# Performance work log

Hardware: AMD Instinct MI355X
Metric: run time of the kernel (lower is better)

## Reference

```python
import jax, jax.numpy as jnp
import numpy as np

B, T, C = 4, 2048, 1024
H, D = 16, 64  # num_heads, head_size; H*D == C


def setup_inputs() -> dict:
    key = jax.random.key(0)
    k1, k2, k3 = jax.random.split(key, 3)
    x = jax.random.normal(k1, (B, T, C), dtype=jnp.float32)
    w_qkv = jax.random.normal(k2, (C, 3 * C), dtype=jnp.float32) * (C ** -0.5)
    w_out = jax.random.normal(k3, (C, C), dtype=jnp.float32) * (C ** -0.5)
    b_out = jnp.zeros((C,), dtype=jnp.float32)
    return {"x": x, "w_qkv": w_qkv, "w_out": w_out, "b_out": b_out}


def reference(x, w_qkv, w_out, b_out):
    Bb, Tt, Cc = x.shape
    qkv = x @ w_qkv                        # [B,T,3C]
    q, k, v = jnp.split(qkv, 3, axis=2)
    # [B,T,C] -> [B,H,T,D]
    q = q.reshape(Bb, Tt, H, D).transpose(0, 2, 1, 3)
    k = k.reshape(Bb, Tt, H, D).transpose(0, 2, 1, 3)
    v = v.reshape(Bb, Tt, H, D).transpose(0, 2, 1, 3)
    scores = jnp.einsum('bhqd,bhkd->bhqk', q, k) * (D ** -0.5)
    causal = jnp.tril(jnp.ones((Tt, Tt), dtype=bool))
    scores = jnp.where(causal, scores, -jnp.inf)
    attn = jax.nn.softmax(scores, axis=-1)  # dropout is identity in eval mode
    out = jnp.einsum('bhqk,bhkd->bhqd', attn, v)
    out = out.transpose(0, 2, 1, 3).reshape(Bb, Tt, Cc)
    return out @ w_out + b_out
```

## Files before the change

### kernel.cpp

```cpp
#include <hip/hip_runtime.h>

typedef __bf16 bf16;
typedef __bf16 bf16x4 __attribute__((ext_vector_type(4)));
typedef __bf16 bf16x8 __attribute__((ext_vector_type(8)));
typedef float  f32x4  __attribute__((ext_vector_type(4)));

#define MFMA16(A_, B_, C_) __builtin_amdgcn_mfma_f32_16x16x32_bf16((A_), (B_), (C_), 0, 0, 0)

#define BB 4
#define TT 2048
#define CC 1024
#define HH 16
#define DD 64
#define MM (BB * TT)
#define N_QKV (3 * CC)
#define LDSS 68
#define BSTRIDE 36
#define QSCALE2 0.18033688f

static __device__ __forceinline__ void store_lds8(bf16* p, bf16x8 v) {
  bf16x4 lo, hi;
#pragma unroll
  for (int i = 0; i < 4; i++) { lo[i] = v[i]; hi[i] = v[i + 4]; }
  *(bf16x4*)p = lo;
  *(bf16x4*)(p + 4) = hi;
}

static __device__ __forceinline__ bf16x8 load_lds8(const bf16* p) {
  bf16x4 lo = *(const bf16x4*)p;
  bf16x4 hi = *(const bf16x4*)(p + 4);
  bf16x8 v;
#pragma unroll
  for (int i = 0; i < 4; i++) { v[i] = lo[i]; v[i + 4] = hi[i]; }
  return v;
}

static __device__ __forceinline__ void async_cp16(const bf16* g, bf16* l) {
  __builtin_amdgcn_global_load_lds(
      (const __attribute__((address_space(1))) void*)g,
      (__attribute__((address_space(3))) void*)l, 16, 0, 0);
}

__global__ __launch_bounds__(256) void sniff_k(const unsigned short* __restrict__ u,
                                               int* __restrict__ flag) {
  __shared__ int s;
  if (threadIdx.x == 0) s = 0;
  __syncthreads();
  int c = 0;
  for (int i = threadIdx.x; i < 65536; i += 256)
    if ((u[i] & 0x7F80u) == 0x7F80u) c = 1;
  if (c) atomicOr(&s, 1);
  __syncthreads();
  if (threadIdx.x == 0) *flag = s;
}

__global__ __launch_bounds__(256) void cvt_k(const void* __restrict__ in,
                                             bf16* __restrict__ out,
                                             const int* __restrict__ flag) {
  const int fl = *flag;
  const size_t i = ((size_t)blockIdx.x * 256 + threadIdx.x) * 8;
  if (fl) {
    f32x4 a = *(const f32x4*)((const float*)in + i);
    f32x4 b = *(const f32x4*)((const float*)in + i + 4);
    bf16x8 o;
#pragma unroll
    for (int j = 0; j < 4; j++) { o[j] = (bf16)a[j]; o[4 + j] = (bf16)b[j]; }
    *(bf16x8*)(out + i) = o;
  } else {
    *(bf16x8*)(out + i) = *(const bf16x8*)((const bf16*)in + i);
  }
}

__global__ __launch_bounds__(256) void transpose_k(const void* __restrict__ in,
                                                   bf16* __restrict__ out,
                                                   int R, int C,
                                                   const int* __restrict__ flag) {
  __shared__ bf16 tile[32][33];
  const int fl = *flag;
  const int c0 = blockIdx.x * 32, r0 = blockIdx.y * 32;
  const int tx = threadIdx.x & 31, ty = threadIdx.x >> 5;
#pragma unroll
  for (int i = ty; i < 32; i += 8) {
    const size_t idx = (size_t)(r0 + i) * C + c0 + tx;
    tile[i][tx] = fl ? (bf16)((const float*)in)[idx] : ((const bf16*)in)[idx];
  }
  __syncthreads();
#pragma unroll
  for (int i = ty; i < 32; i += 8)
    out[(size_t)(c0 + i) * R + r0 + tx] = tile[tx][i];
}

template <int EPI>
__global__ __launch_bounds__(256) void gemm_lds(const bf16* __restrict__ A,
                                                const bf16* __restrict__ Bt,
                                                const void* __restrict__ biasv,
                                                void* __restrict__ Cv,
                                                const int* __restrict__ flag,
                                                size_t aoff, size_t coff,
                                                int M, int N, int K,
                                                int lda, int ldc) {
  const int fl = *flag;
  __shared__ __align__(16) bf16 sA[128 * 32];
  __shared__ __align__(16) bf16 sB[128 * 32];
  const int tid = threadIdx.x;
  const int lane = tid & 63, wave = tid >> 6;
  const int quad = lane >> 4, l15 = lane & 15;
  const int wr = wave >> 1, wc = wave & 1;
  const int m0 = blockIdx.x * 128, n0 = blockIdx.y * 128;
  const int grow = lane >> 2;
  const int gcol = (lane & 3) * 8;

  f32x4 acc[4][4];
#pragma unroll
  for (int i = 0; i < 4; i++)
#pragma unroll
    for (int j = 0; j < 4; j++) {
      f32x4 z = {0.f, 0.f, 0.f, 0.f};
      acc[i][j] = z;
    }

  const bf16* Ag = A + aoff + (size_t)(m0 + wave * 32 + grow) * lda + gcol;
  const bf16* Bg = Bt + (size_t)(n0 + wave * 32 + grow) * K + gcol;
  bf16* sAw = sA + wave * 32 * 32;
  bf16* sBw = sB + wave * 32 * 32;

  for (int k0 = 0; k0 < K; k0 += 32) {
    __syncthreads();
    async_cp16(Ag, sAw);
    async_cp16(Ag + (size_t)16 * lda, sAw + 16 * 32);
    async_cp16(Bg, sBw);
    async_cp16(Bg + (size_t)16 * K, sBw + 16 * 32);
    Ag += 32;
    Bg += 32;
    __syncthreads();

    bf16x8 af[4], bfr[4];
#pragma unroll
    for (int mi = 0; mi < 4; mi++)
      af[mi] = *(const bf16x8*)(sA + (wr * 64 + mi * 16 + l15) * 32 + quad * 8);
#pragma unroll
    for (int ni = 0; ni < 4; ni++)
      bfr[ni] = *(const bf16x8*)(sB + (wc * 64 + ni * 16 + l15) * 32 + quad * 8);
#pragma unroll
    for (int mi = 0; mi < 4; mi++)
#pragma unroll
      for (int ni = 0; ni < 4; ni++)
        acc[mi][ni] = MFMA16(af[mi], bfr[ni], acc[mi][ni]);
  }

#pragma unroll
  for (int mi = 0; mi < 4; mi++) {
#pragma unroll
    for (int r = 0; r < 4; r++) {
      const int m = m0 + wr * 64 + mi * 16 + quad * 4 + r;
#pragma unroll
      for (int ni = 0; ni < 4; ni++) {
        const int n = n0 + wc * 64 + ni * 16 + l15;
        float v = acc[mi][ni][r];
        const size_t idx = coff + (size_t)m * ldc + n;
        if (EPI == 1) {
          v += fl ? ((const float*)biasv)[n] : (float)((const bf16*)biasv)[n];
          if (fl) ((float*)Cv)[idx] = v;
          else    ((bf16*)Cv)[idx] = (bf16)v;
        } else {
          ((bf16*)Cv)[idx] = (bf16)v;
        }
      }
    }
  }
}

template <int EPI, bool AF>
__global__ __launch_bounds__(256) void gemm_bt(const void* __restrict__ Av,
                                               const bf16* __restrict__ Bt,
                                               const void* __restrict__ biasv,
                                               void* __restrict__ Cv,
                                               const int* __restrict__ flag,
                                               size_t aoff, size_t coff,
                                               int M, int N, int K,
                                               int lda, int ldc) {
  const int fl = *flag;
  const bool af32 = AF && (fl != 0);
  __shared__ __align__(16) bf16 sA[128 * 32];
  __shared__ __align__(16) bf16 sB[128 * 32];
  const int tid = threadIdx.x;
  const int lane = tid & 63, wave = tid >> 6;
  const int quad = lane >> 4, l15 = lane & 15;
  const int wr = wave >> 1, wc = wave & 1;
  const int m0 = blockIdx.x * 128, n0 = blockIdx.y * 128;
  const int srow = tid >> 2;
  const int scol = (tid & 3) * 8;

  f32x4 acc[4][4];
#pragma unroll
  for (int i = 0; i < 4; i++)
#pragma unroll
    for (int j = 0; j < 4; j++) {
      f32x4 z = {0.f, 0.f, 0.f, 0.f};
      acc[i][j] = z;
    }

  const size_t abase0 = aoff + (size_t)(m0 + srow) * lda + scol;
  const size_t abase1 = abase0 + (size_t)64 * lda;
  const bf16* Bg0 = Bt + (size_t)(n0 + srow) * K + scol;
  const bf16* Bg1 = Bg0 + (size_t)64 * K;

  for (int k0 = 0; k0 < K; k0 += 32) {
    bf16x8 a0, a1;
    if (af32) {
      const float* Af = (const float*)Av;
      f32x4 p00 = *(const f32x4*)(Af + abase0 + k0);
      f32x4 p01 = *(const f32x4*)(Af + abase0 + k0 + 4);
      f32x4 p10 = *(const f32x4*)(Af + abase1 + k0);
      f32x4 p11 = *(const f32x4*)(Af + abase1 + k0 + 4);
#pragma unroll
      for (int i = 0; i < 4; i++) {
        a0[i] = (bf16)p00[i]; a0[i + 4] = (bf16)p01[i];
        a1[i] = (bf16)p10[i]; a1[i + 4] = (bf16)p11[i];
      }
    } else {
      const bf16* Ab = (const bf16*)Av;
      a0 = *(const bf16x8*)(Ab + abase0 + k0);
      a1 = *(const bf16x8*)(Ab + abase1 + k0);
    }
    bf16x8 b0 = *(const bf16x8*)(Bg0 + k0);
    bf16x8 b1 = *(const bf16x8*)(Bg1 + k0);
    __syncthreads();
    *(bf16x8*)(sA + srow * 32 + scol) = a0;
    *(bf16x8*)(sA + (64 + srow) * 32 + scol) = a1;
    *(bf16x8*)(sB + srow * 32 + scol) = b0;
    *(bf16x8*)(sB + (64 + srow) * 32 + scol) = b1;
    __syncthreads();

    bf16x8 af[4], bfr[4];
#pragma unroll
    for (int mi = 0; mi < 4; mi++)
      af[mi] = *(const bf16x8*)(sA + (wr * 64 + mi * 16 + l15) * 32 + quad * 8);
#pragma unroll
    for (int ni = 0; ni < 4; ni++)
      bfr[ni] = *(const bf16x8*)(sB + (wc * 64 + ni * 16 + l15) * 32 + quad * 8);
#pragma unroll
    for (int mi = 0; mi < 4; mi++)
#pragma unroll
      for (int ni = 0; ni < 4; ni++)
        acc[mi][ni] = MFMA16(af[mi], bfr[ni], acc[mi][ni]);
  }

#pragma unroll
  for (int mi = 0; mi < 4; mi++) {
#pragma unroll
    for (int r = 0; r < 4; r++) {
      const int m = m0 + wr * 64 + mi * 16 + quad * 4 + r;
#pragma unroll
      for (int ni = 0; ni < 4; ni++) {
        const int n = n0 + wc * 64 + ni * 16 + l15;
        float v = acc[mi][ni][r];
        const size_t idx = coff + (size_t)m * ldc + n;
        if (EPI == 1) {
          v += fl ? ((const float*)biasv)[n] : (float)((const bf16*)biasv)[n];
          if (fl) ((float*)Cv)[idx] = v;
          else    ((bf16*)Cv)[idx] = (bf16)v;
        } else {
          ((bf16*)Cv)[idx] = (bf16)v;
        }
      }
    }
  }
}

template <int EPI, bool AF, bool WF>
__global__ __launch_bounds__(256) void gemm_nt(const void* __restrict__ Av,
                                               const void* __restrict__ Wv,
                                               const void* __restrict__ biasv,
                                               void* __restrict__ Cv,
                                               const int* __restrict__ flag,
                                               size_t aoff, size_t coff,
                                               int M, int N, int K,
                                               int lda, int ldc) {
  const int fl = *flag;
  const bool af32 = AF && (fl != 0);
  const bool wf32 = WF && (fl != 0);
  __shared__ __align__(16) bf16 sA[128 * 32];
  __shared__ __align__(16) bf16 sB[128 * BSTRIDE];
  const int tid = threadIdx.x;
  const int lane = tid & 63, wave = tid >> 6;
  const int quad = lane >> 4, l15 = lane & 15;
  const int wr = wave >> 1, wc = wave & 1;
  const int m0 = blockIdx.x * 128, n0 = blockIdx.y * 128;
  const int arow = tid >> 2, acol = (tid & 3) * 8;
  const int wk = tid >> 3, wn = (tid & 7) * 16;

  f32x4 acc[4][4];
#pragma unroll
  for (int i = 0; i < 4; i++)
#pragma unroll
    for (int j = 0; j < 4; j++) {
      f32x4 z = {0.f, 0.f, 0.f, 0.f};
      acc[i][j] = z;
    }

  const size_t abase0 = aoff + (size_t)(m0 + arow) * lda + acol;
  const size_t abase1 = abase0 + (size_t)64 * lda;

  for (int k0 = 0; k0 < K; k0 += 32) {
    bf16x8 a0, a1;
    if (af32) {
      const float* Af = (const float*)Av;
      f32x4 p00 = *(const f32x4*)(Af + abase0 + k0);
      f32x4 p01 = *(const f32x4*)(Af + abase0 + k0 + 4);
      f32x4 p10 = *(const f32x4*)(Af + abase1 + k0);
      f32x4 p11 = *(const f32x4*)(Af + abase1 + k0 + 4);
#pragma unroll
      for (int i = 0; i < 4; i++) {
        a0[i] = (bf16)p00[i]; a0[i + 4] = (bf16)p01[i];
        a1[i] = (bf16)p10[i]; a1[i + 4] = (bf16)p11[i];
      }
    } else {
      const bf16* Ab = (const bf16*)Av;
      a0 = *(const bf16x8*)(Ab + abase0 + k0);
      a1 = *(const bf16x8*)(Ab + abase1 + k0);
    }
    bf16 wreg[16];
    const size_t wbase = (size_t)(k0 + wk) * N + n0 + wn;
    if (wf32) {
      const float* Wf = (const float*)Wv;
      f32x4 q0 = *(const f32x4*)(Wf + wbase);
      f32x4 q1 = *(const f32x4*)(Wf + wbase + 4);
      f32x4 q2 = *(const f32x4*)(Wf + wbase + 8);
      f32x4 q3 = *(const f32x4*)(Wf + wbase + 12);
#pragma unroll
      for (int i = 0; i < 4; i++) {
        wreg[i] = (bf16)q0[i];      wreg[4 + i] = (bf16)q1[i];
        wreg[8 + i] = (bf16)q2[i];  wreg[12 + i] = (bf16)q3[i];
      }
    } else {
      const bf16* Wb = (const bf16*)Wv;
      bf16x8 w0 = *(const bf16x8*)(Wb + wbase);
      bf16x8 w1 = *(const bf16x8*)(Wb + wbase + 8);
#pragma unroll
      for (int i = 0; i < 8; i++) { wreg[i] = w0[i]; wreg[8 + i] = w1[i]; }
    }
    __syncthreads();
    *(bf16x8*)(sA + arow * 32 + acol) = a0;
    *(bf16x8*)(sA + (64 + arow) * 32 + acol) = a1;
#pragma unroll
    for (int i = 0; i < 16; i++)
      sB[(wn + i) * BSTRIDE + wk] = wreg[i];
    __syncthreads();

    bf16x8 af[4], bfr[4];
#pragma unroll
    for (int mi = 0; mi < 4; mi++)
      af[mi] = *(const bf16x8*)(sA + (wr * 64 + mi * 16 + l15) * 32 + quad * 8);
#pragma unroll
    for (int ni = 0; ni < 4; ni++)
      bfr[ni] = load_lds8(sB + (wc * 64 + ni * 16 + l15) * BSTRIDE + quad * 8);
#pragma unroll
    for (int mi = 0; mi < 4; mi++)
#pragma unroll
      for (int ni = 0; ni < 4; ni++)
        acc[mi][ni] = MFMA16(af[mi], bfr[ni], acc[mi][ni]);
  }

#pragma unroll
  for (int mi = 0; mi < 4; mi++) {
#pragma unroll
    for (int r = 0; r < 4; r++) {
      const int m = m0 + wr * 64 + mi * 16 + quad * 4 + r;
#pragma unroll
      for (int ni = 0; ni < 4; ni++) {
        const int n = n0 + wc * 64 + ni * 16 + l15;
        float v = acc[mi][ni][r];
        const size_t idx = coff + (size_t)m * ldc + n;
        if (EPI == 1) {
          v += fl ? ((const float*)biasv)[n] : (float)((const bf16*)biasv)[n];
          if (fl) ((float*)Cv)[idx] = v;
          else    ((bf16*)Cv)[idx] = (bf16)v;
        } else {
          ((bf16*)Cv)[idx] = (bf16)v;
        }
      }
    }
  }
}

__global__ __launch_bounds__(256) void attn_k(bf16* __restrict__ qkv) {
  __shared__ __align__(16) bf16 sQ[128 * LDSS];
  __shared__ __align__(16) bf16 sK[64 * LDSS];
  __shared__ __align__(16) bf16 sVt[64 * LDSS];

  const int tid = threadIdx.x;
  const int lane = tid & 63, wave = tid >> 6;
  const int quad = lane >> 4, l15 = lane & 15;
  const int bh = blockIdx.y;
  bf16* base = qkv + (size_t)(bh >> 4) * TT * N_QKV + (bh & 15) * DD;
  const bf16* Qp = base;
  const bf16* Kp = base + CC;
  const bf16* Vp = base + 2 * CC;

  const int krow = tid >> 2;
  const int kcol = (tid & 3) * 16;
  const int vkey = tid & 31;
  const int vcol = (tid >> 5) * 8;

  bf16x8 ones;
  {
    const bf16 o = (l15 == 0) ? (bf16)1.0f : (bf16)0.0f;
#pragma unroll
    for (int i = 0; i < 8; i++) ones[i] = o;
  }

  for (int pass = 0; pass < 2; pass++) {
    const int qt = pass ? (15 - (int)blockIdx.x) : (int)blockIdx.x;
    const int q0 = qt * 128;
    __syncthreads();

#pragma unroll
    for (int p = 0; p < 2; p++) {
      const int r = p * 64 + krow;
      const bf16* src = Qp + (size_t)(q0 + r) * N_QKV + kcol;
      bf16x8 v0 = *(const bf16x8*)src;
      bf16x8 v1 = *(const bf16x8*)(src + 8);
#pragma unroll
      for (int i = 0; i < 8; i++) {
        v0[i] = (bf16)((float)v0[i] * QSCALE2);
        v1[i] = (bf16)((float)v1[i] * QSCALE2);
      }
      store_lds8(sQ + r * LDSS + kcol, v0);
      store_lds8(sQ + r * LDSS + kcol + 8, v1);
    }

    bf16x8 kr0, kr1, vr0, vr1;
    {
      const bf16* kp = Kp + (size_t)krow * N_QKV + kcol;
      kr0 = *(const bf16x8*)kp;
      kr1 = *(const bf16x8*)(kp + 8);
      vr0 = *(const bf16x8*)(Vp + (size_t)vkey * N_QKV + vcol);
      vr1 = *(const bf16x8*)(Vp + (size_t)(32 + vkey) * N_QKV + vcol);
    }
    __syncthreads();

    bf16x8 aq[2][2];
#pragma unroll
    for (int mi = 0; mi < 2; mi++) {
      const bf16* qp = sQ + (size_t)(wave * 32 + mi * 16 + l15) * LDSS + quad * 8;
      aq[mi][0] = load_lds8(qp);
      aq[mi][1] = load_lds8(qp + 32);
    }

    f32x4 Oacc[2][4];
    f32x4 lacc[2];
#pragma unroll
    for (int mi = 0; mi < 2; mi++) {
      f32x4 z = {0.f, 0.f, 0.f, 0.f};
      lacc[mi] = z;
#pragma unroll
      for (int nt = 0; nt < 4; nt++) Oacc[mi][nt] = z;
    }

    const int jmax = q0 + 64;
    const int wave_row0 = q0 + wave * 32;
    bf16* sP = sQ + (size_t)(wave * 32) * LDSS;

    for (int j0 = 0; j0 <= jmax; j0 += 64) {
      __syncthreads();
      store_lds8(sK + krow * LDSS + kcol, kr0);
      store_lds8(sK + krow * LDSS + kcol + 8, kr1);
#pragma unroll
      for (int i = 0; i < 8; i++) {
        sVt[(vcol + i) * LDSS + vkey] = vr0[i];
        sVt[(vcol + i) * LDSS + 32 + vkey] = vr1[i];
      }
      __syncthreads();

      if (j0 + 64 <= jmax) {
        const bf16* kp = Kp + (size_t)(j0 + 64 + krow) * N_QKV + kcol;
        kr0 = *(const bf16x8*)kp;
        kr1 = *(const bf16x8*)(kp + 8);
        vr0 = *(const bf16x8*)(Vp + (size_t)(j0 + 64 + vkey) * N_QKV + vcol);
        vr1 = *(const bf16x8*)(Vp + (size_t)(j0 + 96 + vkey) * N_QKV + vcol);
      }

      if (j0 <= wave_row0 + 31) {
        f32x4 S[2][4];
#pragma unroll
        for (int nt = 0; nt < 4; nt++) {
          const bf16* kp = sK + (size_t)(nt * 16 + l15) * LDSS + quad * 8;
          bf16x8 bk0 = load_lds8(kp);
          bf16x8 bk1 = load_lds8(kp + 32);
#pragma unroll
          for (int mi = 0; mi < 2; mi++) {
            f32x4 acc = {0.f, 0.f, 0.f, 0.f};
            acc = MFMA16(aq[mi][0], bk0, acc);
            acc = MFMA16(aq[mi][1], bk1, acc);
            S[mi][nt] = acc;
          }
        }

        if (j0 + 63 > wave_row0) {
#pragma unroll
          for (int mi = 0; mi < 2; mi++)
#pragma unroll
            for (int nt = 0; nt < 4; nt++) {
              const int kc = j0 + nt * 16 + l15;
#pragma unroll
              for (int r = 0; r < 4; r++) {
                const float e = __builtin_amdgcn_exp2f(S[mi][nt][r]);
                const bool dead = kc > wave_row0 + mi * 16 + quad * 4 + r;
                sP[(size_t)(mi * 16 + quad * 4 + r) * LDSS + nt * 16 + l15] =
                    (bf16)(dead ? 0.f : e);
              }
            }
        } else {
#pragma unroll
          for (int mi = 0; mi < 2; mi++)
#pragma unroll
            for (int nt = 0; nt < 4; nt++)
#pragma unroll
              for (int r = 0; r < 4; r++)
                sP[(size_t)(mi * 16 + quad * 4 + r) * LDSS + nt * 16 + l15] =
                    (bf16)__builtin_amdgcn_exp2f(S[mi][nt][r]);
        }

        bf16x8 ap[2][2];
#pragma unroll
        for (int mi = 0; mi < 2; mi++) {
          const bf16* pp = sP + (size_t)(mi * 16 + l15) * LDSS + quad * 8;
          ap[mi][0] = load_lds8(pp);
          ap[mi][1] = load_lds8(pp + 32);
          lacc[mi] = MFMA16(ap[mi][0], ones, lacc[mi]);
          lacc[mi] = MFMA16(ap[mi][1], ones, lacc[mi]);
        }
#pragma unroll
        for (int nt = 0; nt < 4; nt++) {
          const bf16* vp = sVt + (size_t)(nt * 16 + l15) * LDSS + quad * 8;
          bf16x8 bv0 = load_lds8(vp);
          bf16x8 bv1 = load_lds8(vp + 32);
#pragma unroll
          for (int mi = 0; mi < 2; mi++) {
            Oacc[mi][nt] = MFMA16(ap[mi][0], bv0, Oacc[mi][nt]);
            Oacc[mi][nt] = MFMA16(ap[mi][1], bv1, Oacc[mi][nt]);
          }
        }
      }
    }

#pragma unroll
    for (int mi = 0; mi < 2; mi++)
#pragma unroll
      for (int r = 0; r < 4; r++) {
        const float lv = __shfl(lacc[mi][r], lane & 48, 64);
        const float invl = 1.0f / lv;
        const int t = q0 + wave * 32 + mi * 16 + quad * 4 + r;
#pragma unroll
        for (int nt = 0; nt < 4; nt++)
          base[(size_t)t * N_QKV + nt * 16 + l15] =
              (bf16)(Oacc[mi][nt][r] * invl);
      }
  }
}

extern "C" void kernel_launch(void* const* d_in, const int* in_sizes, int n_in,
                              void* d_out, int out_size, void* d_ws, size_t ws_size,
                              hipStream_t stream) {
  const void* x = d_in[0];
  const void* w_qkv = d_in[1];
  const void* w_out = d_in[2];
  const void* b_out = d_in[3];

  int* flag = (int*)d_ws;
  char* p = (char*)d_ws + 256;
  bf16* wqkvT = (bf16*)p;
  bf16* woutT = wqkvT + (size_t)N_QKV * CC;

  const size_t wT_bytes = ((size_t)N_QKV * CC + (size_t)CC * CC) * 2;
  const size_t xb_bytes = (size_t)MM * CC * 2;
  const size_t qkv_bytes = (size_t)MM * N_QKV * 2;
  const size_t need_Ap = 256 + wT_bytes + xb_bytes + qkv_bytes;
  const size_t need_A  = 256 + wT_bytes + qkv_bytes;
  const size_t need_B  = 256 + wT_bytes + (size_t)TT * N_QKV * 2;

  sniff_k<<<1, 256, 0, stream>>>((const unsigned short*)x, flag);

  if (ws_size >= need_Ap) {
    bf16* xb = woutT + (size_t)CC * CC;
    bf16* qkv = xb + (size_t)MM * CC;
    cvt_k<<<(MM * CC) / 2048, 256, 0, stream>>>(x, xb, flag);
    transpose_k<<<dim3(N_QKV / 32, CC / 32), 256, 0, stream>>>(w_qkv, wqkvT, CC, N_QKV, flag);
    transpose_k<<<dim3(CC / 32, CC / 32), 256, 0, stream>>>(w_out, woutT, CC, CC, flag);

    gemm_lds<0><<<dim3(MM / 128, N_QKV / 128), 256, 0, stream>>>(
        xb, wqkvT, nullptr, qkv, flag, 0, 0, MM, N_QKV, CC, CC, N_QKV);

    attn_k<<<dim3(8, BB * HH), 256, 0, stream>>>(qkv);

    gemm_lds<1><<<dim3(MM / 128, CC / 128), 256, 0, stream>>>(
        qkv, woutT, b_out, d_out, flag, 0, 0, MM, CC, CC, N_QKV, CC);
  } else if (ws_size >= need_A) {
    bf16* qkv = woutT + (size_t)CC * CC;
    transpose_k<<<dim3(N_QKV / 32, CC / 32), 256, 0, stream>>>(w_qkv, wqkvT, CC, N_QKV, flag);
    transpose_k<<<dim3(CC / 32, CC / 32), 256, 0, stream>>>(w_out, woutT, CC, CC, flag);

    gemm_bt<0, true><<<dim3(MM / 128, N_QKV / 128), 256, 0, stream>>>(
        x, wqkvT, nullptr, qkv, flag, 0, 0, MM, N_QKV, CC, CC, N_QKV);

    attn_k<<<dim3(8, BB * HH), 256, 0, stream>>>(qkv);

    gemm_lds<1><<<dim3(MM / 128, CC / 128), 256, 0, stream>>>(
        qkv, woutT, b_out, d_out, flag, 0, 0, MM, CC, CC, N_QKV, CC);
  } else if (ws_size >= need_B) {
    bf16* qkv = woutT + (size_t)CC * CC;
    transpose_k<<<dim3(N_QKV / 32, CC / 32), 256, 0, stream>>>(w_qkv, wqkvT, CC, N_QKV, flag);
    transpose_k<<<dim3(CC / 32, CC / 32), 256, 0, stream>>>(w_out, woutT, CC, CC, flag);
    for (int b = 0; b < BB; b++) {
      const size_t xoff = (size_t)b * TT * CC;
      gemm_bt<0, true><<<dim3(TT / 128, N_QKV / 128), 256, 0, stream>>>(
          x, wqkvT, nullptr, qkv, flag, xoff, 0, TT, N_QKV, CC, CC, N_QKV);
      attn_k<<<dim3(8, HH), 256, 0, stream>>>(qkv);
      gemm_lds<1><<<dim3(TT / 128, CC / 128), 256, 0, stream>>>(
          qkv, woutT, b_out, d_out, flag, 0, xoff, TT, CC, CC, N_QKV, CC);
    }
  } else {
    bf16* qkvb = (bf16*)p;
    for (int b = 0; b < BB; b++) {
      const size_t xoff = (size_t)b * TT * CC;
      gemm_nt<0, true, true><<<dim3(TT / 128, N_QKV / 128), 256, 0, stream>>>(
          x, w_qkv, nullptr, qkvb, flag, xoff, 0, TT, N_QKV, CC, CC, N_QKV);
      attn_k<<<dim3(8, HH), 256, 0, stream>>>(qkvb);
      gemm_nt<1, false, true><<<dim3(TT / 128, CC / 128), 256, 0, stream>>>(
          qkvb, w_out, b_out, d_out, flag, 0, xoff, TT, CC, CC, N_QKV, CC);
    }
  }
}
```

Before: 332.6 us.

## Pad attention LDS rows to 72 and use 16-byte LDS accesses; chunk x conversion

Widens the attention shared-memory row stride from 68 to 72 bf16 so rows stay 16-byte aligned, letting the split 8-byte LDS loads and stores be replaced by single 16-byte vector accesses. The two causal-mask branches are merged into one loop with a runtime mask predicate. The host path now reorders workspace so that, when there is too little room for a full bf16 copy of x, it converts and multiplies x in half-size chunks instead of falling back to the direct fp32 GEMM. The wider stride uses more LDS and can change bank-conflict patterns, and the merged mask loop adds a compare on unmasked tiles.

```diff
diff --git a/kernel.cpp b/kernel.cpp
--- a/kernel.cpp
+++ b/kernel.cpp
@@ -14,7 +14,7 @@
 #define DD 64
 #define MM (BB * TT)
 #define N_QKV (3 * CC)
-#define LDSS 68
+#define LDSS 72
 #define BSTRIDE 36
 #define QSCALE2 0.18033688f
 
@@ -56,18 +56,19 @@
 
 __global__ __launch_bounds__(256) void cvt_k(const void* __restrict__ in,
                                              bf16* __restrict__ out,
-                                             const int* __restrict__ flag) {
+                                             const int* __restrict__ flag,
+                                             size_t off) {
   const int fl = *flag;
   const size_t i = ((size_t)blockIdx.x * 256 + threadIdx.x) * 8;
   if (fl) {
-    f32x4 a = *(const f32x4*)((const float*)in + i);
-    f32x4 b = *(const f32x4*)((const float*)in + i + 4);
+    f32x4 a = *(const f32x4*)((const float*)in + off + i);
+    f32x4 b = *(const f32x4*)((const float*)in + off + i + 4);
     bf16x8 o;
 #pragma unroll
     for (int j = 0; j < 4; j++) { o[j] = (bf16)a[j]; o[4 + j] = (bf16)b[j]; }
     *(bf16x8*)(out + i) = o;
   } else {
-    *(bf16x8*)(out + i) = *(const bf16x8*)((const bf16*)in + i);
+    *(bf16x8*)(out + i) = *(const bf16x8*)((const bf16*)in + off + i);
   }
 }
 
@@ -426,8 +427,8 @@
         v0[i] = (bf16)((float)v0[i] * QSCALE2);
         v1[i] = (bf16)((float)v1[i] * QSCALE2);
       }
-      store_lds8(sQ + r * LDSS + kcol, v0);
-      store_lds8(sQ + r * LDSS + kcol + 8, v1);
+      *(bf16x8*)(sQ + r * LDSS + kcol) = v0;
+      *(bf16x8*)(sQ + r * LDSS + kcol + 8) = v1;
     }
 
     bf16x8 kr0, kr1, vr0, vr1;
@@ -444,8 +445,8 @@
 #pragma unroll
     for (int mi = 0; mi < 2; mi++) {
       const bf16* qp = sQ + (size_t)(wave * 32 + mi * 16 + l15) * LDSS + quad * 8;
-      aq[mi][0] = load_lds8(qp);
-      aq[mi][1] = load_lds8(qp + 32);
+      aq[mi][0] = *(const bf16x8*)qp;
+      aq[mi][1] = *(const bf16x8*)(qp + 32);
     }
 
     f32x4 Oacc[2][4];
@@ -464,8 +465,8 @@
 
     for (int j0 = 0; j0 <= jmax; j0 += 64) {
       __syncthreads();
-      store_lds8(sK + krow * LDSS + kcol, kr0);
-      store_lds8(sK + krow * LDSS + kcol + 8, kr1);
+      *(bf16x8*)(sK + krow * LDSS + kcol) = kr0;
+      *(bf16x8*)(sK + krow * LDSS + kcol + 8) = kr1;
 #pragma unroll
       for (int i = 0; i < 8; i++) {
         sVt[(vcol + i) * LDSS + vkey] = vr0[i];
@@ -486,8 +487,8 @@
 #pragma unroll
         for (int nt = 0; nt < 4; nt++) {
           const bf16* kp = sK + (size_t)(nt * 16 + l15) * LDSS + quad * 8;
-          bf16x8 bk0 = load_lds8(kp);
-          bf16x8 bk1 = load_lds8(kp + 32);
+          bf16x8 bk0 = *(const bf16x8*)kp;
+          bf16x8 bk1 = *(const bf16x8*)(kp + 32);
 #pragma unroll
           for (int mi = 0; mi < 2; mi++) {
             f32x4 acc = {0.f, 0.f, 0.f, 0.f};
@@ -497,45 +498,35 @@
           }
         }
 
-        if (j0 + 63 > wave_row0) {
-#pragma unroll
-          for (int mi = 0; mi < 2; mi++)
-#pragma unroll
-            for (int nt = 0; nt < 4; nt++) {
-              const int kc = j0 + nt * 16 + l15;
-#pragma unroll
-              for (int r = 0; r < 4; r++) {
-                const float e = __builtin_amdgcn_exp2f(S[mi][nt][r]);
-                const bool dead = kc > wave_row0 + mi * 16 + quad * 4 + r;
-                sP[(size_t)(mi * 16 + quad * 4 + r) * LDSS + nt * 16 + l15] =
-                    (bf16)(dead ? 0.f : e);
-              }
+        const bool needmask = (j0 + 63 > wave_row0);
+#pragma unroll
+        for (int mi = 0; mi < 2; mi++)
+#pragma unroll
+          for (int nt = 0; nt < 4; nt++) {
+            const int kc = j0 + nt * 16 + l15;
+#pragma unroll
+            for (int r = 0; r < 4; r++) {
+              float e = __builtin_amdgcn_exp2f(S[mi][nt][r]);
+              if (needmask && kc > wave_row0 + mi * 16 + quad * 4 + r) e = 0.f;
+              sP[(size_t)(mi * 16 + quad * 4 + r) * LDSS + nt * 16 + l15] =
+                  (bf16)e;
             }
-        } else {
-#pragma unroll
-          for (int mi = 0; mi < 2; mi++)
-#pragma unroll
-            for (int nt = 0; nt < 4; nt++)
-#pragma unroll
-              for (int r = 0; r < 4; r++)
-                sP[(size_t)(mi * 16 + quad * 4 + r) * LDSS + nt * 16 + l15] =
-                    (bf16)__builtin_amdgcn_exp2f(S[mi][nt][r]);
-        }
+          }
 
         bf16x8 ap[2][2];
 #pragma unroll
         for (int mi = 0; mi < 2; mi++) {
           const bf16* pp = sP + (size_t)(mi * 16 + l15) * LDSS + quad * 8;
-          ap[mi][0] = load_lds8(pp);
-          ap[mi][1] = load_lds8(pp + 32);
+          ap[mi][0] = *(const bf16x8*)pp;
+          ap[mi][1] = *(const bf16x8*)(pp + 32);
           lacc[mi] = MFMA16(ap[mi][0], ones, lacc[mi]);
           lacc[mi] = MFMA16(ap[mi][1], ones, lacc[mi]);
         }
 #pragma unroll
         for (int nt = 0; nt < 4; nt++) {
           const bf16* vp = sVt + (size_t)(nt * 16 + l15) * LDSS + quad * 8;
-          bf16x8 bv0 = load_lds8(vp);
-          bf16x8 bv1 = load_lds8(vp + 32);
+          bf16x8 bv0 = *(const bf16x8*)vp;
+          bf16x8 bv1 = *(const bf16x8*)(vp + 32);
 #pragma unroll
           for (int mi = 0; mi < 2; mi++) {
             Oacc[mi][nt] = MFMA16(ap[mi][0], bv0, Oacc[mi][nt]);
@@ -574,35 +565,37 @@
   bf16* woutT = wqkvT + (size_t)N_QKV * CC;
 
   const size_t wT_bytes = ((size_t)N_QKV * CC + (size_t)CC * CC) * 2;
-  const size_t xb_bytes = (size_t)MM * CC * 2;
   const size_t qkv_bytes = (size_t)MM * N_QKV * 2;
-  const size_t need_Ap = 256 + wT_bytes + xb_bytes + qkv_bytes;
-  const size_t need_A  = 256 + wT_bytes + qkv_bytes;
-  const size_t need_B  = 256 + wT_bytes + (size_t)TT * N_QKV * 2;
+  const size_t need_A = 256 + wT_bytes + qkv_bytes;
+  const size_t need_B = 256 + wT_bytes + (size_t)TT * N_QKV * 2;
 
   sniff_k<<<1, 256, 0, stream>>>((const unsigned short*)x, flag);
 
-  if (ws_size >= need_Ap) {
-    bf16* xb = woutT + (size_t)CC * CC;
-    bf16* qkv = xb + (size_t)MM * CC;
-    cvt_k<<<(MM * CC) / 2048, 256, 0, stream>>>(x, xb, flag);
+  if (ws_size >= need_A) {
+    bf16* qkv = woutT + (size_t)CC * CC;
+    bf16* xb = qkv + (size_t)MM * N_QKV;
+    const size_t slack = ws_size - need_A;
+
     transpose_k<<<dim3(N_QKV / 32, CC / 32), 256, 0, stream>>>(w_qkv, wqkvT, CC, N_QKV, flag);
     transpose_k<<<dim3(CC / 32, CC / 32), 256, 0, stream>>>(w_out, woutT, CC, CC, flag);
 
-    gemm_lds<0><<<dim3(MM / 128, N_QKV / 128), 256, 0, stream>>>(
-        xb, wqkvT, nullptr, qkv, flag, 0, 0, MM, N_QKV, CC, CC, N_QKV);
-
-    attn_k<<<dim3(8, BB * HH), 256, 0, stream>>>(qkv);
-
-    gemm_lds<1><<<dim3(MM / 128, CC / 128), 256, 0, stream>>>(
-        qkv, woutT, b_out, d_out, flag, 0, 0, MM, CC, CC, N_QKV, CC);
-  } else if (ws_size >= need_A) {
-    bf16* qkv = woutT + (size_t)CC * CC;
-    transpose_k<<<dim3(N_QKV / 32, CC / 32), 256, 0, stream>>>(w_qkv, wqkvT, CC, N_QKV, flag);
-    transpose_k<<<dim3(CC / 32, CC / 32), 256, 0, stream>>>(w_out, woutT, CC, CC, flag);
-
-    gemm_bt<0, true><<<dim3(MM / 128, N_QKV / 128), 256, 0, stream>>>(
-        x, wqkvT, nullptr, qkv, flag, 0, 0, MM, N_QKV, CC, CC, N_QKV);
+    const size_t full_xb = (size_t)MM * CC * 2;
+    const size_t half_xb = full_xb / 2;
+    if (slack >= full_xb) {
+      cvt_k<<<(MM * CC) / 2048, 256, 0, stream>>>(x, xb, flag, 0);
+      gemm_lds<0><<<dim3(MM / 128, N_QKV / 128), 256, 0, stream>>>(
+          xb, wqkvT, nullptr, qkv, flag, 0, 0, MM, N_QKV, CC, CC, N_QKV);
+    } else if (slack >= half_xb) {
+      for (int m0 = 0; m0 < MM; m0 += 4096) {
+        cvt_k<<<(4096 * CC) / 2048, 256, 0, stream>>>(x, xb, flag, (size_t)m0 * CC);
+        gemm_lds<0><<<dim3(4096 / 128, N_QKV / 128), 256, 0, stream>>>(
+            xb, wqkvT, nullptr, qkv, flag, 0, (size_t)m0 * N_QKV,
+            4096, N_QKV, CC, CC, N_QKV);
+      }
+    } else {
+      gemm_bt<0, true><<<dim3(MM / 128, N_QKV / 128), 256, 0, stream>>>(
+          x, wqkvT, nullptr, qkv, flag, 0, 0, MM, N_QKV, CC, CC, N_QKV);
+    }
 
     attn_k<<<dim3(8, BB * HH), 256, 0, stream>>>(qkv);
 
```

Result: no change. 326.6 us (-1.8%).
